# Kernel optimization log

Measured on AMD Instinct MI355X. Metric: run time of the kernel, lower is better.

The kernel has to match this reference:

```python
import jax, jax.numpy as jnp
import numpy as np
from functools import partial

# Config (BranchNet 'big'-style)
HIST = [42, 78, 150, 294, 582]
PW = [3, 6, 12, 24, 48]
SHIFTING = [False, False, True, True, True]
CW = 7          # conv width
F = 32          # conv filters
E = 32          # embedding dims
B = 4096        # batch
H_TOT = 590     # total history length
V = 8192        # 2**(pc_hash_bits+1)
WBITS = 2       # weight quantization bits
ABITS = 3       # activation quantization bits
EPS = 1e-5


@partial(jax.custom_vjp, nondiff_argnums=(1,))
def quant_signed(x, bits):
    # Quantize.forward (signed, bits>1): round(x*scale)/scale, scale=(1<<(bits-1))-1
    scale = float((1 << (bits - 1)) - 1)
    return jnp.round(x * scale) / scale

def _q_fwd(x, bits):
    return quant_signed(x, bits), None

def _q_bwd(bits, res, g):
    # straight-through estimator, matching Quantize.backward
    return (g,)

quant_signed.defvjp(_q_fwd, _q_bwd)


def batchnorm(x, gamma, beta, axes, pshape):
    # training-mode BatchNorm1d: batch statistics, biased variance
    m = jnp.mean(x, axis=axes, keepdims=True)
    v = jnp.var(x, axis=axes, keepdims=True)
    return gamma.reshape(pshape) * (x - m) * jax.lax.rsqrt(v + EPS) + beta.reshape(pshape)


def extract_slice_history(x, global_shift, slice_size, pooling_width, shifting):
    # vectorized version of the per-sample Python loop in extract_slice_history
    h_tot = x.shape[1]
    if shifting:
        s = jnp.mod(global_shift, pooling_width)              # [B]
        start = (h_tot - s - slice_size)[:, None]             # [B,1]
        idx = start + jnp.arange(slice_size)[None, :]         # [B,L]
        return jnp.take_along_axis(x, idx, axis=1)
    return x[:, -slice_size:]


def fc_layer(x, W, b, gamma, beta):
    # FCLayer with quantized weights + batchnorm + hardtanh + quantized act
    w = quant_signed(jnp.clip(W, -1.0, 1.0), WBITS)
    y = x @ w.T + b
    y = batchnorm(y, gamma, beta, (0,), (1, -1))
    y = jnp.clip(y, -1.0, 1.0)  # hardtanh
    return quant_signed(y, ABITS)


def branchnet_forward(x, global_shift, emb, conv_w, conv_b, bn1_g, bn1_b,
                      bnp_g, bnp_b, W1, b1, g1, be1, W2, b2, g2, be2, W3, b3):
    feats = []
    for i in range(len(HIST)):
        L, pw = HIST[i], PW[i]
        xs = extract_slice_history(x, global_shift, L, pw, SHIFTING[i])  # [B,L] int
        e = jnp.take(emb[i], xs, axis=0)                                 # [B,L,E]
        e = jnp.transpose(e, (0, 2, 1))                                  # [B,E,L]
        h = jax.lax.conv_general_dilated(
            e, conv_w[i], window_strides=(1,), padding='VALID',
            dimension_numbers=('NCH', 'OIH', 'NCH')) + conv_b[i][None, :, None]
        h = batchnorm(h, bn1_g[i], bn1_b[i], (0, 2), (1, -1, 1))
        h = jnp.tanh(h)
        T = (L - CW + 1) // pw                                           # = 12
        p = h[:, :, :T * pw].reshape(h.shape[0], F, T, pw).mean(axis=-1) # AvgPool1d
        p = batchnorm(p, bnp_g[i], bnp_b[i], (0, 2), (1, -1, 1))
        feats.append(p.reshape(p.shape[0], -1))                          # [B, F*T]
    z = jnp.concatenate(feats, axis=1)                                   # [B, 1920]
    z = fc_layer(z, W1, b1, g1, be1)
    z = fc_layer(z, W2, b2, g2, be2)
    w3 = quant_signed(jnp.clip(W3, -1.0, 1.0), WBITS)
    out = z @ w3.T + b3                                                  # [B,1]
    return out[:, 0]                                                     # squeeze(dim=1)


def setup_inputs() -> dict:
    key = jax.random.key(0)
    ks = jax.random.split(key, 12)
    return {
        'x': jax.random.randint(ks[0], (B, H_TOT), 0, V, dtype=jnp.int32),
        'global_shift': jax.random.randint(ks[1], (B,), 0, 48, dtype=jnp.int32),
        'emb': jax.random.normal(ks[2], (5, V, E), jnp.float32) * 0.1,
        'conv_w': jax.random.normal(ks[3], (5, F, E, CW), jnp.float32) * 0.1,
        'conv_b': jax.random.normal(ks[4], (5, F), jnp.float32) * 0.01,
        'bn1_g': jnp.ones((5, F), jnp.float32),
        'bn1_b': jnp.zeros((5, F), jnp.float32),
        'bnp_g': jnp.ones((5, F), jnp.float32),
        'bnp_b': jnp.zeros((5, F), jnp.float32),
        'W1': jax.random.uniform(ks[5], (2048, 1920), jnp.float32, -1.0, 1.0),
        'b1': jax.random.normal(ks[6], (2048,), jnp.float32) * 0.01,
        'g1': jnp.ones((2048,), jnp.float32),
        'be1': jnp.zeros((2048,), jnp.float32),
        'W2': jax.random.uniform(ks[7], (2048, 2048), jnp.float32, -1.0, 1.0),
        'b2': jax.random.normal(ks[8], (2048,), jnp.float32) * 0.01,
        'g2': jnp.ones((2048,), jnp.float32),
        'be2': jnp.zeros((2048,), jnp.float32),
        'W3': jax.random.uniform(ks[9], (1, 2048), jnp.float32, -1.0, 1.0),
        'b3': jax.random.normal(ks[10], (1,), jnp.float32) * 0.01,
    }


def reference(x, global_shift, emb, conv_w, conv_b, bn1_g, bn1_b, bnp_g, bnp_b,
              W1, b1, g1, be1, W2, b2, g2, be2, W3, b3):
    return branchnet_forward(x, global_shift, emb, conv_w, conv_b, bn1_g, bn1_b,
                             bnp_g, bnp_b, W1, b1, g1, be1, W2, b2, g2, be2, W3, b3)
```

## Files before the change

### kernel.cpp

```cpp
#include <hip/hip_runtime.h>
#include <cmath>

#define HTOT  590
#define BATCH 4096
#define VOCAB 8192

typedef _Float16 f16;
typedef __attribute__((ext_vector_type(8))) _Float16 f16x8;
typedef __attribute__((ext_vector_type(4))) _Float16 f16x4;
typedef __attribute__((ext_vector_type(4))) float f32x4;
typedef __attribute__((ext_vector_type(16))) float f32x16;

constexpr size_t OFF_EHL  = 0;
constexpr size_t OFF_WF   = 1310720;
constexpr size_t OFF_PA   = 1364480;
constexpr size_t OFF_PB   = 2937344;
constexpr size_t OFF_BN1  = 4510208;
constexpr size_t OFF_BNP  = 4510528;
constexpr size_t OFF_CP   = 4510848;
constexpr size_t OFF_BNF1 = 4641920;
constexpr size_t OFF_PRAW = 4646016;
constexpr size_t OFF_W1P  = 12510336;
constexpr size_t OFF_W2P  = 14476416;
constexpr size_t OFF_Y    = 16573568;
constexpr size_t OFF_BNF2 = 24962176;
constexpr size_t OFF_Z2K  = 0;
constexpr size_t OFF_Z3K  = 4194304;

__device__ __forceinline__ float qw(float w) {
  return rintf(fminf(fmaxf(w, -1.f), 1.f));
}
__device__ __forceinline__ float4 ld4(const float* p) {
  return *reinterpret_cast<const float4*>(p);
}
__device__ __forceinline__ float tanh_c(float u) {
  const float e = __expf(2.f*u);
  return 1.f - __fdividef(2.f, e + 1.f);
}

#define MF(A,B,C) __builtin_amdgcn_mfma_f32_32x32x16_f16(A,B,C,0,0,0)
#define WV(K,KS,V) (*reinterpret_cast<const f16x8*>(wfsl + (((K)*2+(KS))*3+(V))*256 + lane*4))

__global__ __launch_bounds__(256) void k_eprep(const float* __restrict__ emb,
                                               f16* __restrict__ ehl)
{
  const int idx = blockIdx.x*256 + threadIdx.x;
  const int c = idx & 31, v = (idx >> 5) & 8191, slice = idx >> 18;
  const float val = emb[(size_t)(slice*VOCAB + v)*32 + c];
  const f16 hi = (f16)val;
  const f16 lo = (f16)((val - (float)hi)*2048.f);
  f16* row = ehl + (size_t)(slice*VOCAB + v)*64;
  row[c] = hi; row[32 + c] = lo;
}

__global__ __launch_bounds__(256) void k_wfprep(const float* __restrict__ convw,
                                                f16* __restrict__ wf)
{
  const int idx = blockIdx.x*256 + threadIdx.x;
  const int j = idx & 7, lane = (idx >> 3) & 63;
  const int rest = idx >> 9;
  const int v = rest % 3;
  const int rest2 = rest / 3;
  const int ks = rest2 & 1, kk = rest2 >> 1;
  const int k = kk % 7, slice = kk / 7;
  const int f = lane & 31, c = ks*16 + (lane >> 5)*8 + j;
  const float val = convw[((slice*32 + f)*32 + c)*7 + k];
  const f16 hi = (f16)val;
  f16 o;
  if (v == 0)      o = (f16)((float)hi * 2048.f);
  else if (v == 1) o = (f16)((val - (float)hi)*2048.f);
  else             o = hi;
  wf[idx] = o;
}

template<int PASS>
__global__ __launch_bounds__(256, 4) void k_convm(const int* __restrict__ x,
                                                  const int* __restrict__ gshift,
                                                  const float* __restrict__ ehl,
                                                  const float* __restrict__ wfrag,
                                                  const float* __restrict__ bn1,
                                                  float* __restrict__ z,
                                                  float* __restrict__ partials)
{
  const int b = blockIdx.x;
  const int type = blockIdx.y;
  const int tid = threadIdx.x;
  const int wid = tid >> 6, lane = tid & 63;
  const int lt = lane & 31, hf = lane >> 5;

  __shared__ float smem[9408];
  __shared__ int   tokid[294];

  float* tokarr = smem;
  f16*   hstat  = (f16*)smem;
  float* part2  = smem + 6000;
  float* thbuf  = smem;
  float* poolb  = smem + 4224;

  const int gsv = gshift[b];
  const int NTOK = (type == 0) ? 270 : 294;

  for (int i = tid; i < NTOK; i += 256) {
    int xs, q = i;
    if (type == 0) {
      if (i < 42)       { xs = 548; }
      else if (i < 120) { xs = 512; q = i - 42; }
      else              { xs = 440 - gsv % 12; q = i - 120; }
    } else if (type == 1) xs = 296 - gsv % 24;
    else if (type == 2)   xs = 8 - gsv % 48;
    else                  xs = 8 - gsv % 48 + 288;
    int xi = xs + q; if (xi < 0) xi += HTOT;
    tokid[i] = x[b*HTOT + xi];
  }
  __syncthreads();
  for (int j = tid; j < NTOK*8; j += 256) {
    const int row = j >> 3, ch = j & 7;
    const int sl = (type == 0) ? (row < 42 ? 0 : (row < 120 ? 1 : 2)) : ((type == 1) ? 3 : 4);
    const float4 v = ld4(ehl + (size_t)(sl*VOCAB + tokid[row])*32 + ch*4);
    *reinterpret_cast<float4*>(&tokarr[ch*1176 + row*4]) = v;
  }
  __syncthreads();

  int slice, tb, nt, slotoff, ThV, pw, si;
  if (type == 0) {
    if      (wid == 0) { slice=0; tb=0;  nt=2; slotoff=0;   ThV=36;  pw=3;  si=0; }
    else if (wid == 1) { slice=1; tb=0;  nt=3; slotoff=42;  ThV=72;  pw=6;  si=1; }
    else if (wid == 2) { slice=2; tb=0;  nt=3; slotoff=120; ThV=144; pw=12; si=2; }
    else               { slice=2; tb=96; nt=2; slotoff=120; ThV=144; pw=12; si=2; }
  } else if (type == 1) {
    slice=3; pw=24; ThV=288; slotoff=0; si=0;
    tb = (wid == 0) ? 0 : 32 + wid*64; nt = (wid == 0) ? 3 : 2;
  } else if (type == 2) {
    slice=4; pw=48; ThV=288; slotoff=0; si=0;
    tb = (wid == 0) ? 0 : 32 + wid*64; nt = (wid == 0) ? 3 : 2;
  } else {
    slice=4; pw=48; ThV=576; slotoff=-288; si=0;
    tb = 288 + ((wid == 0) ? 0 : 32 + wid*64); nt = (wid == 0) ? 3 : 2;
  }
  const int wb = (type == 3) ? 6 : 0;
  const int slot0 = (type == 0) ? ((wid == 0) ? 0 : (wid == 1) ? 2 : (wid == 2) ? 5 : 8)
                                : ((wid == 0) ? 0 : 1 + wid*2);

  const float* wfsl = wfrag + slice*10752;

  f32x16 acc[3];
  #pragma unroll
  for (int r = 0; r < 3; ++r)
    #pragma unroll
    for (int i = 0; i < 16; ++i) acc[r][i] = 0.f;

  const float* pb = tokarr + hf*1176 + (size_t)(slotoff + tb + lt)*4;
  #pragma unroll 1
  for (int k = 0; k < 7; ++k) {
    const f16x8 wh2_0 = WV(k,0,0), wl_0 = WV(k,0,1), wh_0 = WV(k,0,2);
    const f16x8 wh2_1 = WV(k,1,0), wl_1 = WV(k,1,1), wh_1 = WV(k,1,2);
    #pragma unroll
    for (int r = 0; r < 3; ++r) if (r < nt) {
      const float* rp = pb + k*4 + r*128;
      const f16x8 bh0 = *(const f16x8*)(rp);
      const f16x8 bh1 = *(const f16x8*)(rp + 2352);
      const f16x8 bl0 = *(const f16x8*)(rp + 4704);
      const f16x8 bl1 = *(const f16x8*)(rp + 7056);
      acc[r] = MF(wh2_0, bh0, acc[r]);
      acc[r] = MF(wl_0,  bh0, acc[r]);
      acc[r] = MF(wh_0,  bl0, acc[r]);
      acc[r] = MF(wh2_1, bh1, acc[r]);
      acc[r] = MF(wl_1,  bh1, acc[r]);
      acc[r] = MF(wh_1,  bl1, acc[r]);
    }
  }
  __syncthreads();

  if (PASS == 0) {
    #pragma unroll
    for (int r = 0; r < 3; ++r) if (r < nt) {
      const int tbg = tb + r*32;
      const int slot = slot0 + r;
      #pragma unroll
      for (int i = 0; i < 16; ++i) {
        const int fr = (i&3) + 8*(i>>2) + 4*hf;
        const float h = acc[r][i]*(1.f/2048.f);
        const float hv = (tbg + lt < ThV) ? h : 0.f;
        hstat[slot*1088 + fr*34 + lt] = (f16)hv;
      }
    }
    __syncthreads();
    const int nslot = (type == 0) ? 10 : 9;
    for (int j = tid; j < nslot*32; j += 256) {
      const int slot = j >> 5, f = j & 31;
      const f16* rowp = hstat + slot*1088 + f*34;
      float s1 = 0.f, s2 = 0.f;
      #pragma unroll
      for (int t = 0; t < 32; ++t) { const float v = (float)rowp[t]; s1 += v; s2 += v*v; }
      part2[(slot*32 + f)*2]     = s1;
      part2[(slot*32 + f)*2 + 1] = s2;
    }
    __syncthreads();
    const int nch = (type == 0) ? 96 : 32;
    if (tid < nch) {
      const int sic = tid >> 5, f = tid & 31;
      int slo, shi, Pb;
      if (type == 0) {
        slo = (sic == 0) ? 0 : (sic == 1) ? 2 : 5;
        shi = (sic == 0) ? 2 : (sic == 1) ? 5 : 10;
        Pb  = sic*32;
      } else { slo = 0; shi = 9; Pb = 96 + (type - 1)*32; }
      float s1 = 0.f, s2 = 0.f;
      for (int s = slo; s < shi; ++s) {
        s1 += part2[(s*32 + f)*2];
        s2 += part2[(s*32 + f)*2 + 1];
      }
      partials[(size_t)b*384 + (Pb + f)*2]     = s1;
      partials[(size_t)b*384 + (Pb + f)*2 + 1] = s2;
    }
    return;
  }

  for (int i = tid; i < 2304; i += 256) poolb[i] = 0.f;
  __syncthreads();

  float A1v[16], B1v[16];
  #pragma unroll
  for (int i = 0; i < 16; ++i) {
    const int fr = (i&3) + 8*(i>>2) + 4*hf;
    A1v[i] = bn1[slice*32 + fr];
    B1v[i] = bn1[160 + slice*32 + fr];
  }

  #pragma unroll
  for (int r = 0; r < 3; ++r) if (r < nt) {
    const int tbg = tb + r*32;
    #pragma unroll
    for (int i = 0; i < 16; ++i) {
      const int fr = (i&3) + 8*(i>>2) + 4*hf;
      const float h = acc[r][i]*(1.f/2048.f);
      thbuf[wid*1056 + fr*33 + lt] = tanh_c(A1v[i]*h + B1v[i]);
    }
    const int tvend = min(tbg + 32, ThV);
    const int wlo = tbg / pw, whi = (tvend - 1) / pw;
    for (int w = wlo; w <= whi; ++w) {
      const int lo = max(w*pw, tbg), hi2 = min((w+1)*pw, tvend);
      float s = 0.f;
      for (int t = lo + hf; t < hi2; t += 2) s += thbuf[wid*1056 + lt*33 + (t - tbg)];
      s += __shfl_xor(s, 32);
      if (hf == 0) {
        const int piece = (w*pw < tbg) ? 1 : 0;
        poolb[(si*12 + (w - wb))*64 + piece*32 + lt] = s;
      }
    }
  }
  __syncthreads();

  const int nch = (type == 0) ? 96 : 32;
  if (tid < nch) {
    const int sic = tid >> 5, f = tid & 31;
    const int sg = (type == 0) ? sic : ((type == 1) ? 3 : 4);
    const int P = (sg < 4) ? sg*32 + f : ((type == 2) ? 128 + f : 160 + f);
    const int pwc = (type == 0) ? ((sic == 0) ? 3 : (sic == 1) ? 6 : 12)
                                : ((type == 1) ? 24 : 48);
    const int nwin = (type >= 2) ? 6 : 12;
    const int wbc = (type == 3) ? 6 : 0;
    const float inv = 1.f/(float)pwc;
    float s1 = 0.f, s2 = 0.f;
    for (int wl = 0; wl < nwin; ++wl) {
      const float p = (poolb[(sic*12 + wl)*64 + f] + poolb[(sic*12 + wl)*64 + 32 + f]) * inv;
      z[(size_t)b*1920 + sg*384 + (wl + wbc)*32 + f] = p;
      s1 += p; s2 += p*p;
    }
    partials[(size_t)b*384 + P*2]     = s1;
    partials[(size_t)b*384 + P*2 + 1] = s2;
  }
}

template<int PASS>
__global__ __launch_bounds__(256) void k_bnfinal(const float* __restrict__ partials,
                                                 const float* __restrict__ gamma,
                                                 const float* __restrict__ beta,
                                                 float* __restrict__ outAB)
{
  const int c = blockIdx.x;
  const int slice = c >> 5, f = c & 31;
  const int tid = threadIdx.x;
  double s1 = 0.0, s2 = 0.0;
  for (int b = tid; b < BATCH; b += 256) {
    const float* p = partials + (size_t)b*384;
    if (slice < 4) { s1 += p[(slice*32+f)*2]; s2 += p[(slice*32+f)*2+1]; }
    else {
      s1 += (double)p[(128+f)*2]   + (double)p[(160+f)*2];
      s2 += (double)p[(128+f)*2+1] + (double)p[(160+f)*2+1];
    }
  }
  __shared__ double r1[256], r2[256];
  r1[tid] = s1; r2[tid] = s2;
  __syncthreads();
  for (int off = 128; off > 0; off >>= 1) {
    if (tid < off) { r1[tid] += r1[tid+off]; r2[tid] += r2[tid+off]; }
    __syncthreads();
  }
  if (tid == 0) {
    long N;
    if (PASS == 0) { const long Tall[5] = {36,72,144,288,576}; N = (long)BATCH * Tall[slice]; }
    else           { N = (long)BATCH * 12; }
    const double m   = r1[0]/(double)N;
    const double var = r2[0]/(double)N - m*m;
    const float rstd = (float)(1.0/sqrt(var + 1e-5));
    const float Aa = gamma[c]*rstd;
    outAB[c]       = Aa;
    outAB[160 + c] = beta[c] - Aa*(float)m;
  }
}

__global__ __launch_bounds__(256) void k_znorm(float* __restrict__ zz,
                                               const float* __restrict__ bnp)
{
  const size_t i4 = (size_t)blockIdx.x*256 + threadIdx.x;
  const float4 v = ld4(zz + i4*4);
  const int j = (int)((i4*4) % 1920);
  const int slice = j / 384, f0 = j & 31;
  const float4 A = ld4(bnp + slice*32 + f0);
  const float4 B = ld4(bnp + 160 + slice*32 + f0);
  const float zn[4] = {v.x*A.x+B.x, v.y*A.y+B.y, v.z*A.z+B.z, v.w*A.w+B.w};
  uint4 pk;
  unsigned w[4];
  #pragma unroll
  for (int e = 0; e < 4; ++e) {
    const f16 hi = (f16)zn[e];
    const f16 lo = (f16)(zn[e] - (float)hi);
    w[e] = (unsigned)__builtin_bit_cast(unsigned short, hi)
         | ((unsigned)__builtin_bit_cast(unsigned short, lo) << 16);
  }
  pk.x = w[0]; pk.y = w[1]; pk.z = w[2]; pk.w = w[3];
  *reinterpret_cast<uint4*>(zz + i4*4) = pk;
}

__global__ __launch_bounds__(256) void k_wprep1(const float* __restrict__ W1,
                                                f16* __restrict__ W1p)
{
  const int idx = blockIdx.x*256 + threadIdx.x;
  const int n = idx / 1920, klds = idx - n*1920;
  const int slice = klds / 384, r = klds - slice*384;
  const int tp = r >> 5, f = r & 31;
  W1p[idx] = (f16)qw(W1[n*1920 + slice*384 + f*12 + tp]);
}

__global__ __launch_bounds__(256) void k_wprep2(const float* __restrict__ W2,
                                                f16* __restrict__ W2p)
{
  const size_t i4 = (size_t)blockIdx.x*256 + threadIdx.x;
  const float4 v = ld4(W2 + i4*4);
  f16x4 o;
  o[0] = (f16)qw(v.x); o[1] = (f16)qw(v.y); o[2] = (f16)qw(v.z); o[3] = (f16)qw(v.w);
  *reinterpret_cast<f16x4*>(&W2p[i4*4]) = o;
}

template<int SPLIT, int PACKED>
__global__ __launch_bounds__(256) void k_mfgemm(const f16* __restrict__ Ahi,
                                               const unsigned* __restrict__ Apk,
                                               const f16* __restrict__ Bp,
                                               float* __restrict__ C,
                                               const int K, const float oscale)
{
  __shared__ f16 sA[(SPLIT+1)*128][40];
  __shared__ f16 sB[128][40];
  const int tid = threadIdx.x;
  const int bm = blockIdx.y*128, bn = blockIdx.x*128;
  const int wid = tid >> 6, lane = tid & 63;
  const int wm = (wid >> 1)*64, wn = (wid & 1)*64;
  const int lgrp = lane >> 4, lrow = lane & 15;
  f32x4 acc[4][4];
  #pragma unroll
  for (int m = 0; m < 4; ++m)
    #pragma unroll
    for (int n = 0; n < 4; ++n) acc[m][n] = (f32x4){0.f,0.f,0.f,0.f};

  const int srow = tid >> 2, sc = (tid & 3)*8;
  for (int k0 = 0; k0 < K; k0 += 32) {
    #pragma unroll
    for (int u = 0; u < 2; ++u) {
      const int row = srow + u*64;
      if (PACKED) {
        const unsigned* ap = Apk + (size_t)(bm+row)*K + k0 + sc;
        const uint4 v0 = *reinterpret_cast<const uint4*>(ap);
        const uint4 v1 = *reinterpret_cast<const uint4*>(ap + 4);
        uint4 hi, lo;
        hi.x = (v0.x & 0xffffu) | (v0.y << 16);  hi.y = (v0.z & 0xffffu) | (v0.w << 16);
        hi.z = (v1.x & 0xffffu) | (v1.y << 16);  hi.w = (v1.z & 0xffffu) | (v1.w << 16);
        lo.x = (v0.x >> 16) | (v0.y & 0xffff0000u);  lo.y = (v0.z >> 16) | (v0.w & 0xffff0000u);
        lo.z = (v1.x >> 16) | (v1.y & 0xffff0000u);  lo.w = (v1.z >> 16) | (v1.w & 0xffff0000u);
        *reinterpret_cast<uint4*>(&sA[row][sc])     = hi;
        *reinterpret_cast<uint4*>(&sA[128+row][sc]) = lo;
      } else {
        const uint4 va = *reinterpret_cast<const uint4*>(&Ahi[(size_t)(bm+row)*K + k0 + sc]);
        *reinterpret_cast<uint4*>(&sA[row][sc]) = va;
      }
      const uint4 vb = *reinterpret_cast<const uint4*>(&Bp[(size_t)(bn+row)*K + k0 + sc]);
      *reinterpret_cast<uint4*>(&sB[row][sc]) = vb;
    }
    __syncthreads();
    f16x8 bf[4];
    #pragma unroll
    for (int n = 0; n < 4; ++n)
      bf[n] = *reinterpret_cast<const f16x8*>(&sB[wn + n*16 + lrow][lgrp*8]);
    #pragma unroll
    for (int m = 0; m < 4; ++m) {
      const f16x8 ah = *reinterpret_cast<const f16x8*>(&sA[wm + m*16 + lrow][lgrp*8]);
      #pragma unroll
      for (int n = 0; n < 4; ++n)
        acc[m][n] = __builtin_amdgcn_mfma_f32_16x16x32_f16(ah, bf[n], acc[m][n], 0, 0, 0);
      if (SPLIT) {
        const f16x8 al = *reinterpret_cast<const f16x8*>(&sA[128 + wm + m*16 + lrow][lgrp*8]);
        #pragma unroll
        for (int n = 0; n < 4; ++n)
          acc[m][n] = __builtin_amdgcn_mfma_f32_16x16x32_f16(al, bf[n], acc[m][n], 0, 0, 0);
      }
    }
    __syncthreads();
  }
  #pragma unroll
  for (int m = 0; m < 4; ++m)
    #pragma unroll
    for (int n = 0; n < 4; ++n) {
      const int col = bn + wn + n*16 + lrow;
      #pragma unroll
      for (int r = 0; r < 4; ++r)
        C[(size_t)(bm + wm + m*16 + lgrp*4 + r)*2048 + col] = acc[m][n][r]*oscale;
    }
}

__global__ __launch_bounds__(256) void k_colpart(const float* __restrict__ Y,
                                                 double* __restrict__ part, int N)
{
  const int c0 = blockIdx.x*64;
  const int chunk = blockIdx.y;
  const int tid = threadIdx.x;
  const int c = tid & 63, rq = tid >> 6;
  double s1 = 0.0, s2 = 0.0;
  const int rbase = chunk*256;
  for (int r = rbase + rq; r < rbase+256; r += 4) {
    const float v = Y[(size_t)r*N + c0 + c];
    s1 += (double)v; s2 += (double)v*(double)v;
  }
  __shared__ double r1[256], r2[256];
  r1[tid] = s1; r2[tid] = s2;
  __syncthreads();
  if (tid < 64) {
    const double a  = r1[tid]+r1[tid+64]+r1[tid+128]+r1[tid+192];
    const double cc = r2[tid]+r2[tid+64]+r2[tid+128]+r2[tid+192];
    part[(size_t)(c0+c)*32 + chunk*2]     = a;
    part[(size_t)(c0+c)*32 + chunk*2 + 1] = cc;
  }
}

__global__ __launch_bounds__(256) void k_colfinal(const double* __restrict__ part,
                                                  const float* __restrict__ gamma,
                                                  const float* __restrict__ beta,
                                                  float* __restrict__ bnfc, int N)
{
  const int c = blockIdx.x*256 + threadIdx.x;
  if (c >= N) return;
  double s1 = 0.0, s2 = 0.0;
  #pragma unroll
  for (int ch = 0; ch < 16; ++ch) {
    s1 += part[(size_t)c*32 + ch*2];
    s2 += part[(size_t)c*32 + ch*2 + 1];
  }
  const double m   = s1/4096.0;
  const double var = s2/4096.0 - m*m;
  const float rstd = (float)(1.0/sqrt(var + 1e-5));
  const float Aa = gamma[c]*rstd;
  bnfc[c]        = Aa;
  bnfc[2048 + c] = beta[c] - Aa*(float)m;
}

__global__ __launch_bounds__(256) void k_act(const float* __restrict__ Y,
                                             const float* __restrict__ bnfc,
                                             f16* __restrict__ Zk)
{
  const size_t i4 = (size_t)blockIdx.x*256 + threadIdx.x;
  const int cbase = (int)((i4*4) & 2047);
  const float4 v = ld4(Y + i4*4);
  const float4 A = ld4(bnfc + cbase);
  const float4 B = ld4(bnfc + 2048 + cbase);
  const float t[4] = {v.x*A.x+B.x, v.y*A.y+B.y, v.z*A.z+B.z, v.w*A.w+B.w};
  f16x4 o;
  #pragma unroll
  for (int e = 0; e < 4; ++e) {
    const float c = fminf(fmaxf(t[e], -1.f), 1.f);
    o[e] = (f16)rintf(c*3.f);
  }
  *reinterpret_cast<f16x4*>(&Zk[i4*4]) = o;
}

__global__ __launch_bounds__(256) void k_final(const f16* __restrict__ Z3,
                                               const float* __restrict__ W3,
                                               const float* __restrict__ b3,
                                               float* __restrict__ out)
{
  const int b = blockIdx.x;
  const int tid = threadIdx.x;
  float s = 0.f;
  for (int j = tid; j < 2048; j += 256)
    s += (float)Z3[(size_t)b*2048 + j] * qw(W3[j]);
  __shared__ float red[256];
  red[tid] = s;
  __syncthreads();
  for (int off = 128; off > 0; off >>= 1) {
    if (tid < off) red[tid] += red[tid+off];
    __syncthreads();
  }
  if (tid == 0) out[b] = red[0]*(1.f/3.f) + b3[0];
}

extern "C" void kernel_launch(void* const* d_in, const int* in_sizes, int n_in,
                              void* d_out, int out_size, void* d_ws, size_t ws_size,
                              hipStream_t stream)
{
  const int*   x    = (const int*)d_in[0];
  const int*   gs   = (const int*)d_in[1];
  const float* emb  = (const float*)d_in[2];
  const float* cw   = (const float*)d_in[3];
  const float* bn1g = (const float*)d_in[5];
  const float* bn1b = (const float*)d_in[6];
  const float* bnpg = (const float*)d_in[7];
  const float* bnpb = (const float*)d_in[8];
  const float* W1   = (const float*)d_in[9];
  const float* g1   = (const float*)d_in[11];
  const float* be1  = (const float*)d_in[12];
  const float* W2   = (const float*)d_in[13];
  const float* g2   = (const float*)d_in[15];
  const float* be2  = (const float*)d_in[16];
  const float* W3   = (const float*)d_in[17];
  const float* b3   = (const float*)d_in[18];
  float* ws  = (float*)d_ws;
  float* out = (float*)d_out;

  k_eprep<<<5120, 256, 0, stream>>>(emb, (f16*)(ws + OFF_EHL));
  k_wfprep<<<420, 256, 0, stream>>>(cw, (f16*)(ws + OFF_WF));

  k_convm<0><<<dim3(BATCH, 4), 256, 0, stream>>>(x, gs, ws + OFF_EHL, ws + OFF_WF,
                                                 ws + OFF_BN1, nullptr, ws + OFF_PA);
  k_bnfinal<0><<<160, 256, 0, stream>>>(ws + OFF_PA, bn1g, bn1b, ws + OFF_BN1);
  k_convm<1><<<dim3(BATCH, 4), 256, 0, stream>>>(x, gs, ws + OFF_EHL, ws + OFF_WF,
                                                 ws + OFF_BN1, ws + OFF_PRAW, ws + OFF_PB);
  k_bnfinal<1><<<160, 256, 0, stream>>>(ws + OFF_PB, bnpg, bnpb, ws + OFF_BNP);
  k_znorm<<<7680, 256, 0, stream>>>(ws + OFF_PRAW, ws + OFF_BNP);
  k_wprep1<<<15360, 256, 0, stream>>>(W1, (f16*)(ws + OFF_W1P));
  k_wprep2<<<4096, 256, 0, stream>>>(W2, (f16*)(ws + OFF_W2P));

  k_mfgemm<1,1><<<dim3(16, 32), 256, 0, stream>>>(nullptr, (const unsigned*)(ws + OFF_PRAW),
                                                  (const f16*)(ws + OFF_W1P),
                                                  ws + OFF_Y, 1920, 1.f);
  k_colpart<<<dim3(32, 16), 256, 0, stream>>>(ws + OFF_Y, (double*)(ws + OFF_CP), 2048);
  k_colfinal<<<8, 256, 0, stream>>>((const double*)(ws + OFF_CP), g1, be1, ws + OFF_BNF1, 2048);
  k_act<<<8192, 256, 0, stream>>>(ws + OFF_Y, ws + OFF_BNF1, (f16*)(ws + OFF_Z2K));

  k_mfgemm<0,0><<<dim3(16, 32), 256, 0, stream>>>((const f16*)(ws + OFF_Z2K), nullptr,
                                                  (const f16*)(ws + OFF_W2P),
                                                  ws + OFF_Y, 2048, 1.f/3.f);
  k_colpart<<<dim3(32, 16), 256, 0, stream>>>(ws + OFF_Y, (double*)(ws + OFF_CP), 2048);
  k_colfinal<<<8, 256, 0, stream>>>((const double*)(ws + OFF_CP), g2, be2, ws + OFF_BNF2, 2048);
  k_act<<<8192, 256, 0, stream>>>(ws + OFF_Y, ws + OFF_BNF2, (f16*)(ws + OFF_Z3K));

  k_final<<<4096, 256, 0, stream>>>((const f16*)(ws + OFF_Z3K), W3, b3, out);
}
```

Before: 806.5 us.

## Cache conv outputs between passes and fuse column statistics into GEMM epilogue

The first conv pass now writes its pre-BN conv outputs to a workspace buffer as packed hi/lo fp16 pairs, for the slice types that fit. The second pass then reloads them instead of re-gathering embeddings and redoing the MFMA convolution. The FC GEMMs now compute per-column sum and sum-of-squares partials in their epilogue, which removes the separate k_colpart pass over Y. The token gather also pads to a fixed row count with a different smem layout. The cost is a large extra workspace write and read per batch element, and the column stats are now accumulated in fp32 before the double-precision final reduction.

Result: slower. 855.1 us (+6.0%).

```diff
diff --git a/kernel.cpp b/kernel.cpp
--- a/kernel.cpp
+++ b/kernel.cpp
@@ -26,6 +26,7 @@
 constexpr size_t OFF_BNF2 = 24962176;
 constexpr size_t OFF_Z2K  = 0;
 constexpr size_t OFF_Z3K  = 4194304;
+constexpr size_t OFF_H    = 24966272;
 
 __device__ __forceinline__ float qw(float w) {
   return rintf(fminf(fmaxf(w, -1.f), 1.f));
@@ -80,13 +81,16 @@
                                                   const float* __restrict__ wfrag,
                                                   const float* __restrict__ bn1,
                                                   float* __restrict__ z,
-                                                  float* __restrict__ partials)
+                                                  float* __restrict__ partials,
+                                                  unsigned* __restrict__ hbuf,
+                                                  const int hmask, const int NT)
 {
   const int b = blockIdx.x;
   const int type = blockIdx.y;
   const int tid = threadIdx.x;
   const int wid = tid >> 6, lane = tid & 63;
   const int lt = lane & 31, hf = lane >> 5;
+  const bool myH = (hmask >> type) & 1;
 
   __shared__ float smem[9408];
   __shared__ int   tokid[294];
@@ -100,26 +104,33 @@
   const int gsv = gshift[b];
   const int NTOK = (type == 0) ? 270 : 294;
 
-  for (int i = tid; i < NTOK; i += 256) {
-    int xs, q = i;
-    if (type == 0) {
-      if (i < 42)       { xs = 548; }
-      else if (i < 120) { xs = 512; q = i - 42; }
-      else              { xs = 440 - gsv % 12; q = i - 120; }
-    } else if (type == 1) xs = 296 - gsv % 24;
-    else if (type == 2)   xs = 8 - gsv % 48;
-    else                  xs = 8 - gsv % 48 + 288;
-    int xi = xs + q; if (xi < 0) xi += HTOT;
-    tokid[i] = x[b*HTOT + xi];
-  }
-  __syncthreads();
-  for (int j = tid; j < NTOK*8; j += 256) {
-    const int row = j >> 3, ch = j & 7;
-    const int sl = (type == 0) ? (row < 42 ? 0 : (row < 120 ? 1 : 2)) : ((type == 1) ? 3 : 4);
-    const float4 v = ld4(ehl + (size_t)(sl*VOCAB + tokid[row])*32 + ch*4);
-    *reinterpret_cast<float4*>(&tokarr[ch*1176 + row*4]) = v;
-  }
-  __syncthreads();
+  if (!(PASS == 1 && myH)) {
+    for (int i = tid; i < 294; i += 256) {
+      int tok = 0;
+      if (i < NTOK) {
+        int xs, q = i;
+        if (type == 0) {
+          if (i < 42)       { xs = 548; }
+          else if (i < 120) { xs = 512; q = i - 42; }
+          else              { xs = 440 - gsv % 12; q = i - 120; }
+        } else if (type == 1) xs = 296 - gsv % 24;
+        else if (type == 2)   xs = 8 - gsv % 48;
+        else                  xs = 8 - gsv % 48 + 288;
+        int xi = xs + q; if (xi < 0) xi += HTOT;
+        tok = x[b*HTOT + xi];
+      }
+      tokid[i] = tok;
+    }
+    __syncthreads();
+    for (int j = tid; j < 2352; j += 256) {
+      const int ch = j / 294;
+      const int row = j - ch*294;
+      const int sl = (type == 0) ? (row < 42 ? 0 : (row < 120 ? 1 : 2)) : ((type == 1) ? 3 : 4);
+      const float4 v = ld4(ehl + (size_t)(sl*VOCAB + tokid[row])*32 + ch*4);
+      *reinterpret_cast<float4*>(&tokarr[j*4]) = v;
+    }
+    __syncthreads();
+  }
 
   int slice, tb, nt, slotoff, ThV, pw, si;
   if (type == 0) {
@@ -140,6 +151,7 @@
   const int wb = (type == 3) ? 6 : 0;
   const int slot0 = (type == 0) ? ((wid == 0) ? 0 : (wid == 1) ? 2 : (wid == 2) ? 5 : 8)
                                 : ((wid == 0) ? 0 : 1 + wid*2);
+  const int tb2 = (type == 2) ? 0 : ((type == 3) ? 9 : 18);
 
   const float* wfsl = wfrag + slice*10752;
 
@@ -149,24 +161,26 @@
     #pragma unroll
     for (int i = 0; i < 16; ++i) acc[r][i] = 0.f;
 
-  const float* pb = tokarr + hf*1176 + (size_t)(slotoff + tb + lt)*4;
-  #pragma unroll 1
-  for (int k = 0; k < 7; ++k) {
-    const f16x8 wh2_0 = WV(k,0,0), wl_0 = WV(k,0,1), wh_0 = WV(k,0,2);
-    const f16x8 wh2_1 = WV(k,1,0), wl_1 = WV(k,1,1), wh_1 = WV(k,1,2);
-    #pragma unroll
-    for (int r = 0; r < 3; ++r) if (r < nt) {
-      const float* rp = pb + k*4 + r*128;
-      const f16x8 bh0 = *(const f16x8*)(rp);
-      const f16x8 bh1 = *(const f16x8*)(rp + 2352);
-      const f16x8 bl0 = *(const f16x8*)(rp + 4704);
-      const f16x8 bl1 = *(const f16x8*)(rp + 7056);
-      acc[r] = MF(wh2_0, bh0, acc[r]);
-      acc[r] = MF(wl_0,  bh0, acc[r]);
-      acc[r] = MF(wh_0,  bl0, acc[r]);
-      acc[r] = MF(wh2_1, bh1, acc[r]);
-      acc[r] = MF(wl_1,  bh1, acc[r]);
-      acc[r] = MF(wh_1,  bl1, acc[r]);
+  if (!(PASS == 1 && myH)) {
+    const float* pb = tokarr + hf*1176 + (size_t)(slotoff + tb + lt)*4;
+    #pragma unroll 1
+    for (int k = 0; k < 7; ++k) {
+      const f16x8 wh2_0 = WV(k,0,0), wl_0 = WV(k,0,1), wh_0 = WV(k,0,2);
+      const f16x8 wh2_1 = WV(k,1,0), wl_1 = WV(k,1,1), wh_1 = WV(k,1,2);
+      #pragma unroll
+      for (int r = 0; r < 3; ++r) if (r < nt) {
+        const float* rp = pb + k*4 + r*128;
+        const f16x8 bh0 = *(const f16x8*)(rp);
+        const f16x8 bh1 = *(const f16x8*)(rp + 2352);
+        const f16x8 bl0 = *(const f16x8*)(rp + 4704);
+        const f16x8 bl1 = *(const f16x8*)(rp + 7056);
+        acc[r] = MF(wh2_0, bh0, acc[r]);
+        acc[r] = MF(wl_0,  bh0, acc[r]);
+        acc[r] = MF(wh_0,  bl0, acc[r]);
+        acc[r] = MF(wh2_1, bh1, acc[r]);
+        acc[r] = MF(wl_1,  bh1, acc[r]);
+        acc[r] = MF(wh_1,  bl1, acc[r]);
+      }
     }
   }
   __syncthreads();
@@ -176,10 +190,17 @@
     for (int r = 0; r < 3; ++r) if (r < nt) {
       const int tbg = tb + r*32;
       const int slot = slot0 + r;
+      unsigned* hd = hbuf + ((size_t)b*NT + tb2 + slot)*1024 + lt;
       #pragma unroll
       for (int i = 0; i < 16; ++i) {
         const int fr = (i&3) + 8*(i>>2) + 4*hf;
         const float h = acc[r][i]*(1.f/2048.f);
+        if (myH) {
+          const f16 hi = (f16)h;
+          const f16 lo = (f16)((h - (float)hi)*2048.f);
+          hd[fr*32] = (unsigned)__builtin_bit_cast(unsigned short, hi)
+                    | ((unsigned)__builtin_bit_cast(unsigned short, lo) << 16);
+        }
         const float hv = (tbg + lt < ThV) ? h : 0.f;
         hstat[slot*1088 + fr*34 + lt] = (f16)hv;
       }
@@ -230,10 +251,19 @@
   #pragma unroll
   for (int r = 0; r < 3; ++r) if (r < nt) {
     const int tbg = tb + r*32;
+    const unsigned* hs = hbuf + ((size_t)b*NT + tb2 + slot0 + r)*1024 + lt;
     #pragma unroll
     for (int i = 0; i < 16; ++i) {
       const int fr = (i&3) + 8*(i>>2) + 4*hf;
-      const float h = acc[r][i]*(1.f/2048.f);
+      float h;
+      if (myH) {
+        const unsigned w = hs[fr*32];
+        const f16 hi = __builtin_bit_cast(f16, (unsigned short)(w & 0xffffu));
+        const f16 lo = __builtin_bit_cast(f16, (unsigned short)(w >> 16));
+        h = (float)hi + (float)lo*(1.f/2048.f);
+      } else {
+        h = acc[r][i]*(1.f/2048.f);
+      }
       thbuf[wid*1056 + fr*33 + lt] = tanh_c(A1v[i]*h + B1v[i]);
     }
     const int tvend = min(tbg + 32, ThV);
@@ -358,10 +388,12 @@
                                                const unsigned* __restrict__ Apk,
                                                const f16* __restrict__ Bp,
                                                float* __restrict__ C,
+                                               float* __restrict__ cpart,
                                                const int K, const float oscale)
 {
   __shared__ f16 sA[(SPLIT+1)*128][40];
   __shared__ f16 sB[128][40];
+  __shared__ float cst[4][4][16][2];
   const int tid = threadIdx.x;
   const int bm = blockIdx.y*128, bn = blockIdx.x*128;
   const int wid = tid >> 6, lane = tid & 63;
@@ -416,42 +448,40 @@
     }
     __syncthreads();
   }
+  float s1[4] = {0,0,0,0}, s2[4] = {0,0,0,0};
   #pragma unroll
   for (int m = 0; m < 4; ++m)
     #pragma unroll
     for (int n = 0; n < 4; ++n) {
       const int col = bn + wn + n*16 + lrow;
       #pragma unroll
-      for (int r = 0; r < 4; ++r)
-        C[(size_t)(bm + wm + m*16 + lgrp*4 + r)*2048 + col] = acc[m][n][r]*oscale;
-    }
-}
-
-__global__ __launch_bounds__(256) void k_colpart(const float* __restrict__ Y,
-                                                 double* __restrict__ part, int N)
-{
-  const int c0 = blockIdx.x*64;
-  const int chunk = blockIdx.y;
-  const int tid = threadIdx.x;
-  const int c = tid & 63, rq = tid >> 6;
-  double s1 = 0.0, s2 = 0.0;
-  const int rbase = chunk*256;
-  for (int r = rbase + rq; r < rbase+256; r += 4) {
-    const float v = Y[(size_t)r*N + c0 + c];
-    s1 += (double)v; s2 += (double)v*(double)v;
-  }
-  __shared__ double r1[256], r2[256];
-  r1[tid] = s1; r2[tid] = s2;
+      for (int r = 0; r < 4; ++r) {
+        const float v = acc[m][n][r]*oscale;
+        C[(size_t)(bm + wm + m*16 + lgrp*4 + r)*2048 + col] = v;
+        s1[n] += v; s2[n] += v*v;
+      }
+    }
+  #pragma unroll
+  for (int n = 0; n < 4; ++n) {
+    s1[n] += __shfl_xor(s1[n], 16); s1[n] += __shfl_xor(s1[n], 32);
+    s2[n] += __shfl_xor(s2[n], 16); s2[n] += __shfl_xor(s2[n], 32);
+  }
+  if (lgrp == 0) {
+    #pragma unroll
+    for (int n = 0; n < 4; ++n) { cst[wid][n][lrow][0] = s1[n]; cst[wid][n][lrow][1] = s2[n]; }
+  }
   __syncthreads();
-  if (tid < 64) {
-    const double a  = r1[tid]+r1[tid+64]+r1[tid+128]+r1[tid+192];
-    const double cc = r2[tid]+r2[tid+64]+r2[tid+128]+r2[tid+192];
-    part[(size_t)(c0+c)*32 + chunk*2]     = a;
-    part[(size_t)(c0+c)*32 + chunk*2 + 1] = cc;
-  }
-}
-
-__global__ __launch_bounds__(256) void k_colfinal(const double* __restrict__ part,
+  if (tid < 128) {
+    const int n = tid >> 5, half = (tid >> 4) & 1, lr = tid & 15;
+    const float a1 = cst[half][n][lr][0] + cst[half+2][n][lr][0];
+    const float a2 = cst[half][n][lr][1] + cst[half+2][n][lr][1];
+    const int col = bn + half*64 + n*16 + lr;
+    cpart[(size_t)col*64 + blockIdx.y*2]     = a1;
+    cpart[(size_t)col*64 + blockIdx.y*2 + 1] = a2;
+  }
+}
+
+__global__ __launch_bounds__(256) void k_colfinal(const float* __restrict__ part,
                                                   const float* __restrict__ gamma,
                                                   const float* __restrict__ beta,
                                                   float* __restrict__ bnfc, int N)
@@ -460,9 +490,9 @@
   if (c >= N) return;
   double s1 = 0.0, s2 = 0.0;
   #pragma unroll
-  for (int ch = 0; ch < 16; ++ch) {
-    s1 += part[(size_t)c*32 + ch*2];
-    s2 += part[(size_t)c*32 + ch*2 + 1];
+  for (int ch = 0; ch < 32; ++ch) {
+    s1 += (double)part[(size_t)c*64 + ch*2];
+    s2 += (double)part[(size_t)c*64 + ch*2 + 1];
   }
   const double m   = s1/4096.0;
   const double var = s2/4096.0 - m*m;
@@ -534,14 +564,22 @@
   float* ws  = (float*)d_ws;
   float* out = (float*)d_out;
 
+  const bool h23 = ws_size >= (size_t)(OFF_H + 4096ull*18*1024) * 4ull;
+  const bool h1  = h23 && ws_size >= (size_t)(OFF_H + 4096ull*27*1024) * 4ull;
+  const int hmask = (h23 ? 0xC : 0) | (h1 ? 0x2 : 0);
+  const int NT = h1 ? 27 : 18;
+  unsigned* hbuf = (unsigned*)(ws + OFF_H);
+
   k_eprep<<<5120, 256, 0, stream>>>(emb, (f16*)(ws + OFF_EHL));
   k_wfprep<<<420, 256, 0, stream>>>(cw, (f16*)(ws + OFF_WF));
 
   k_convm<0><<<dim3(BATCH, 4), 256, 0, stream>>>(x, gs, ws + OFF_EHL, ws + OFF_WF,
-                                                 ws + OFF_BN1, nullptr, ws + OFF_PA);
+                                                 ws + OFF_BN1, nullptr, ws + OFF_PA,
+                                                 hbuf, hmask, NT);
   k_bnfinal<0><<<160, 256, 0, stream>>>(ws + OFF_PA, bn1g, bn1b, ws + OFF_BN1);
   k_convm<1><<<dim3(BATCH, 4), 256, 0, stream>>>(x, gs, ws + OFF_EHL, ws + OFF_WF,
-                                                 ws + OFF_BN1, ws + OFF_PRAW, ws + OFF_PB);
+                                                 ws + OFF_BN1, ws + OFF_PRAW, ws + OFF_PB,
+                                                 hbuf, hmask, NT);
   k_bnfinal<1><<<160, 256, 0, stream>>>(ws + OFF_PB, bnpg, bnpb, ws + OFF_BNP);
   k_znorm<<<7680, 256, 0, stream>>>(ws + OFF_PRAW, ws + OFF_BNP);
   k_wprep1<<<15360, 256, 0, stream>>>(W1, (f16*)(ws + OFF_W1P));
@@ -549,16 +587,14 @@
 
   k_mfgemm<1,1><<<dim3(16, 32), 256, 0, stream>>>(nullptr, (const unsigned*)(ws + OFF_PRAW),
                                                   (const f16*)(ws + OFF_W1P),
-                                                  ws + OFF_Y, 1920, 1.f);
-  k_colpart<<<dim3(32, 16), 256, 0, stream>>>(ws + OFF_Y, (double*)(ws + OFF_CP), 2048);
-  k_colfinal<<<8, 256, 0, stream>>>((const double*)(ws + OFF_CP), g1, be1, ws + OFF_BNF1, 2048);
+                                                  ws + OFF_Y, ws + OFF_CP, 1920, 1.f);
+  k_colfinal<<<8, 256, 0, stream>>>(ws + OFF_CP, g1, be1, ws + OFF_BNF1, 2048);
   k_act<<<8192, 256, 0, stream>>>(ws + OFF_Y, ws + OFF_BNF1, (f16*)(ws + OFF_Z2K));
 
   k_mfgemm<0,0><<<dim3(16, 32), 256, 0, stream>>>((const f16*)(ws + OFF_Z2K), nullptr,
                                                   (const f16*)(ws + OFF_W2P),
-                                                  ws + OFF_Y, 2048, 1.f/3.f);
-  k_colpart<<<dim3(32, 16), 256, 0, stream>>>(ws + OFF_Y, (double*)(ws + OFF_CP), 2048);
-  k_colfinal<<<8, 256, 0, stream>>>((const double*)(ws + OFF_CP), g2, be2, ws + OFF_BNF2, 2048);
+                                                  ws + OFF_Y, ws + OFF_CP, 2048, 1.f/3.f);
+  k_colfinal<<<8, 256, 0, stream>>>(ws + OFF_CP, g2, be2, ws + OFF_BNF2, 2048);
   k_act<<<8192, 256, 0, stream>>>(ws + OFF_Y, ws + OFF_BNF2, (f16*)(ws + OFF_Z3K));
 
   k_final<<<4096, 256, 0, stream>>>((const f16*)(ws + OFF_Z3K), W3, b3, out);
```
